# Performance work log

Hardware: AMD Instinct MI355X
Metric: run time of the kernel (lower is better)

Reference implementation:

```python
import jax, jax.numpy as jnp
import numpy as np

B, C, H, W = 16, 256, 32, 32
K = 8192            # codebook_size
COMMITMENT = 0.25   # commitment_cost


def setup_inputs() -> dict:
    key = jax.random.key(0)
    k1, k2 = jax.random.split(key)
    z = jax.random.normal(k1, (B, C, H, W), dtype=jnp.float32)
    # matches nn.init.uniform_(codebook.weight, -1/K, 1/K)
    codebook = jax.random.uniform(k2, (K, C), dtype=jnp.float32,
                                  minval=-1.0 / K, maxval=1.0 / K)
    return {"z": z, "codebook": codebook}


def reference(z, codebook):
    b, c, h, w = z.shape
    # (B, C, H, W) -> (B, H*W, C)
    z_flat = z.transpose(0, 2, 3, 1).reshape(b, h * w, c)
    # squared euclidean distances; argmin of sq-dist == argmin of cdist
    z_sq = jnp.sum(z_flat * z_flat, axis=-1, keepdims=True)        # (B, N, 1)
    e_sq = jnp.sum(codebook * codebook, axis=-1)                   # (K,)
    cross = jnp.einsum('bnc,kc->bnk', z_flat, codebook)            # (B, N, K)
    distances = z_sq - 2.0 * cross + e_sq                          # (B, N, K)
    codes = jnp.argmin(distances, axis=-1)                         # (B, N)
    quantized = codebook[codes]                                    # (B, N, C)
    codebook_loss = jnp.mean((quantized - jax.lax.stop_gradient(z_flat)) ** 2)
    commitment_loss = jnp.mean((z_flat - jax.lax.stop_gradient(quantized)) ** 2)
    vq_loss = codebook_loss + COMMITMENT * commitment_loss
    # straight-through estimator
    quantized_st = z_flat + jax.lax.stop_gradient(quantized - z_flat)
    codes_out = codes.reshape(b, h, w)
    quantized_out = quantized_st.reshape(b, h, w, c).transpose(0, 3, 1, 2)
    return codes_out, quantized_out, vq_loss
```

## Files before the change

### kernel.cpp

```cpp
#include <hip/hip_runtime.h>


typedef _Float16 f16;
typedef __attribute__((ext_vector_type(8))) _Float16 f16x8;
typedef __attribute__((ext_vector_type(4))) float f32x4;

#define NPIX   16384
#define CDIM   256
#define KCODE  8192

__global__ void k_prep(const float* __restrict__ z, const float* __restrict__ cb,
                       f16* __restrict__ zhi, f16* __restrict__ zlo,
                       float* __restrict__ zsq,
                       f16* __restrict__ bfh, f16* __restrict__ bfl,
                       float* __restrict__ esq) {
  int bid = blockIdx.x;
  int t   = threadIdx.x;
  if (bid < 512) {
    int kb = bid;
#pragma unroll
    for (int half = 0; half < 2; ++half) {
      int o    = half * 256 + t;
      int lane = o & 63;
      int cs   = o >> 6;
      int code = kb * 16 + (lane & 15);
      int c0   = cs * 32 + ((lane >> 4) & 3) * 8;
      const float* src = cb + (size_t)code * CDIM + c0;
      float4 v0 = *(const float4*)(src);
      float4 v1 = *(const float4*)(src + 4);
      float e[8] = {v0.x, v0.y, v0.z, v0.w, v1.x, v1.y, v1.z, v1.w};
      f16x8 h8, l8;
#pragma unroll
      for (int j = 0; j < 8; ++j) {
        float ej = e[j] * 8192.0f;
        f16 h = (f16)ej;
        h8[j] = h;
        l8[j] = (f16)((ej - (float)h) * 4096.0f);
      }
      size_t off = ((size_t)kb * 512 + o) * 8;
      *(f16x8*)(bfh + off) = h8;
      *(f16x8*)(bfl + off) = l8;
    }
  } else if (bid < 576) {
#pragma clang fp contract(off)
    int n = (bid - 512) * 256 + t;
    int b = n >> 10, p = n & 1023;
    const float* src = z + (size_t)b * CDIM * 1024 + p;
    f16* dh = zhi + (size_t)n * CDIM;
    f16* dl = zlo + (size_t)n * CDIM;
    float half_[2];
    for (int m = 0; m < 2; ++m) {
      float r[8];
#pragma unroll
      for (int j = 0; j < 8; ++j) r[j] = 0.0f;
      for (int i = 0; i < 16; ++i) {
        f16x8 h8, l8;
#pragma unroll
        for (int j = 0; j < 8; ++j) {
          float v = src[(size_t)(m * 128 + i * 8 + j) * 1024];
          r[j] = r[j] + v * v;
          f16 h = (f16)v;
          h8[j] = h;
          l8[j] = (f16)((v - (float)h) * 4096.0f);
        }
        *(f16x8*)(dh + m * 128 + i * 8) = h8;
        *(f16x8*)(dl + m * 128 + i * 8) = l8;
      }
      half_[m] = ((r[0] + r[1]) + (r[2] + r[3])) + ((r[4] + r[5]) + (r[6] + r[7]));
    }
    zsq[n] = half_[0] + half_[1];
  } else {
#pragma clang fp contract(off)
    int row = (bid - 576) * 256 + t;
    const float* src = cb + (size_t)row * CDIM;
    float half_[2];
    for (int m = 0; m < 2; ++m) {
      float r[8];
#pragma unroll
      for (int j = 0; j < 8; ++j) r[j] = 0.0f;
      for (int i = 0; i < 16; ++i) {
        float4 v0 = *(const float4*)(src + m * 128 + i * 8);
        float4 v1 = *(const float4*)(src + m * 128 + i * 8 + 4);
        r[0] = r[0] + v0.x * v0.x;  r[1] = r[1] + v0.y * v0.y;
        r[2] = r[2] + v0.z * v0.z;  r[3] = r[3] + v0.w * v0.w;
        r[4] = r[4] + v1.x * v1.x;  r[5] = r[5] + v1.y * v1.y;
        r[6] = r[6] + v1.z * v1.z;  r[7] = r[7] + v1.w * v1.w;
      }
      half_[m] = ((r[0] + r[1]) + (r[2] + r[3])) + ((r[4] + r[5]) + (r[6] + r[7]));
    }
    esq[row] = half_[0] + half_[1];
  }
}

#define LOADB(Bset, it) do {                                                  \
    int kbq_ = kslice * 64 + (it) * 2 + wk;                                   \
    size_t base_ = (size_t)kbq_ * 4096 + (size_t)lane * 8;                    \
    _Pragma("unroll")                                                         \
    for (int cs_ = 0; cs_ < 8; ++cs_) {                                       \
      Bset[2*cs_]   = *(const f16x8*)(bfh + base_ + (size_t)cs_ * 512);       \
      Bset[2*cs_+1] = *(const f16x8*)(bfl + base_ + (size_t)cs_ * 512);       \
    } } while (0)

#define COMPUTE(Bset, it) do {                                                \
    int kbase_ = kslice * 1024 + (it) * 32 + wk * 16;                         \
    f32x4 hh[2], mx[2];                                                       \
    _Pragma("unroll")                                                         \
    for (int rt = 0; rt < 2; ++rt) { hh[rt] = vzero; mx[rt] = vzero; }        \
    _Pragma("unroll")                                                         \
    for (int cs = 0; cs < 8; ++cs) {                                          \
      f16x8 ah[2], al[2];                                                     \
      _Pragma("unroll")                                                       \
      for (int rt = 0; rt < 2; ++rt) {                                        \
        int px = wh * 32 + rt * 16 + l15;                                     \
        int sb = (cs * 4 + quad) ^ (px & 7);                                  \
        int eo = px * 256 + sb * 8;                            \
        ah[rt] = *(const f16x8*)(sAh + eo);                                   \
        al[rt] = *(const f16x8*)(sAl + eo);                                   \
      }                                                                       \
      _Pragma("unroll")                                                       \
      for (int rt = 0; rt < 2; ++rt) {                                        \
        hh[rt] = __builtin_amdgcn_mfma_f32_16x16x32_f16(ah[rt], Bset[2*cs],   hh[rt], 0, 0, 0); \
        mx[rt] = __builtin_amdgcn_mfma_f32_16x16x32_f16(ah[rt], Bset[2*cs+1], mx[rt], 0, 0, 0); \
        mx[rt] = __builtin_amdgcn_mfma_f32_16x16x32_f16(al[rt], Bset[2*cs],   mx[rt], 0, 0, 0); \
      }                                                                       \
    }                                                                         \
    {                                                                         \
      int k = kbase_ + l15;                                                   \
      float es = esq[k];                                                      \
      _Pragma("unroll")                                                       \
      for (int rt = 0; rt < 2; ++rt)                                          \
        _Pragma("unroll")                                                     \
        for (int rr = 0; rr < 4; ++rr) {                                      \
          float v = hh[rt][rr] * 2.44140625e-4f;                   \
          float w = fmaf(mx[rt][rr], 5.9604644775390625e-8f, v);              \
          float d = (Zr[rt * 4 + rr] - w) + es;                               \
          int j = rt * 4 + rr;                                                \
          if (d < bs[j]) { bs[j] = d; bi[j] = k; }                            \
        }                                                                     \
    } } while (0)

__launch_bounds__(256)
__global__ void k_score(const f16* __restrict__ bfh, const f16* __restrict__ bfl,
                        const f16* __restrict__ zhi, const f16* __restrict__ zlo,
                        const float* __restrict__ esq, const float* __restrict__ zsq,
                        int* __restrict__ cnt,
                        unsigned long long* __restrict__ best) {
  extern __shared__ char smem[];
  f16* sAh = (f16*)smem;
  f16* sAl = (f16*)(smem + 32768);
  int t = threadIdx.x;
  int wave = t >> 6, lane = t & 63;
  int quad = lane >> 4, l15 = lane & 15;
  int wh = wave & 1;
  int wk = wave >> 1;

  __shared__ int s_job[2];
  if (t == 0) {
    unsigned xcc;
    asm volatile("s_getreg_b32 %0, hwreg(HW_REG_XCC_ID)" : "=s"(xcc));
    int x = (int)(xcc & 7u);
    int pt = -1, ks = 0;
    for (int trial = 0; trial < 16 && pt < 0; ++trial) {
      int j = (x + trial) & 7;
      int tk = atomicAdd(&cnt[j], 1);
      if (tk < 256) { pt = tk; ks = j; }
    }
    if (pt < 0) pt = 0;
    s_job[0] = pt; s_job[1] = ks;
  }
  __syncthreads();
  int ptile  = s_job[0];
  int kslice = s_job[1];
  int p0 = ptile * 64;

  {
    int r = t >> 2, seg = t & 3;
    const uint4* gh = (const uint4*)zhi + ((size_t)(p0 + r)) * 32;
    const uint4* gl = (const uint4*)zlo + ((size_t)(p0 + r)) * 32;
    uint4* sh = (uint4*)sAh + r * 32;
    uint4* sl = (uint4*)sAl + r * 32;
#pragma unroll
    for (int j = 0; j < 8; ++j) {
      int blk = seg * 8 + j;
      int sb = blk ^ (r & 7);
      sh[sb] = gh[blk];
      sl[sb] = gl[blk];
    }
  }

  float Zr[8];
#pragma unroll
  for (int rt = 0; rt < 2; ++rt)
#pragma unroll
    for (int rr = 0; rr < 4; ++rr)
      Zr[rt * 4 + rr] = zsq[p0 + wh * 32 + rt * 16 + quad * 4 + rr];

  __syncthreads();

  float bs[8];
  int   bi[8];
#pragma unroll
  for (int j = 0; j < 8; ++j) { bs[j] = 3.0e38f; bi[j] = 0; }

  const f32x4 vzero = {0.0f, 0.0f, 0.0f, 0.0f};

  f16x8 B0[16], B1[16];
  LOADB(B0, 0);
#pragma unroll 1
  for (int tt = 0; tt < 16; ++tt) {
    int i0 = tt * 2, i1 = tt * 2 + 1;
    LOADB(B1, i1);
    COMPUTE(B0, i0);
    int inext = (i1 + 1 < 32) ? i1 + 1 : 31;
    LOADB(B0, inext);
    COMPUTE(B1, i1);
  }

  __syncthreads();
  unsigned long long* red = (unsigned long long*)smem;
#pragma unroll
  for (int j = 0; j < 8; ++j) {
    float s = bs[j]; int i_ = bi[j];
#pragma unroll
    for (int m = 1; m <= 8; m <<= 1) {
      float s2 = __shfl_xor(s, m);
      int   i2 = __shfl_xor(i_, m);
      if (s2 < s || (s2 == s && i2 < i_)) { s = s2; i_ = i2; }
    }
    if (l15 == 0) {
      int row32 = ((j >> 2) << 4) + (quad << 2) + (j & 3);
      unsigned u = __float_as_uint(s);
      u = (u & 0x80000000u) ? ~u : (u | 0x80000000u);
      red[wave * 32 + row32] = ((unsigned long long)u << 32) | (unsigned)i_;
    }
  }
  __syncthreads();
  if (wave == 0) {
    int wh2 = lane >> 5, r31 = lane & 31;
    unsigned long long a = red[wh2 * 32 + r31];
    unsigned long long b = red[(wh2 + 2) * 32 + r31];
    if (b < a) a = b;
    atomicMin(&best[p0 + lane], a);
  }
}

__global__ void k_gather(const float* __restrict__ z, const float* __restrict__ cb,
                         const unsigned long long* __restrict__ best,
                         float* __restrict__ out_codes, float* __restrict__ out_q,
                         float* __restrict__ lossac) {
  int b  = blockIdx.x >> 4;
  int cg = blockIdx.x & 15;
  int t  = threadIdx.x;
  int idx[4];
#pragma unroll
  for (int pi = 0; pi < 4; ++pi) {
    int p = t + pi * 256;
    unsigned long long pk = best[b * 1024 + p];
    idx[pi] = (int)(unsigned)(pk & 0xffffffffu);
    if (cg == 0) out_codes[b * 1024 + p] = (float)idx[pi];
  }
  float lsum = 0.0f;
#pragma unroll
  for (int ci = 0; ci < 16; ++ci) {
    int c = cg * 16 + ci;
#pragma unroll
    for (int pi = 0; pi < 4; ++pi) {
      int p = t + pi * 256;
      float q  = cb[(size_t)idx[pi] * CDIM + c];
      size_t o = ((size_t)(b * CDIM + c)) * 1024 + p;
      float zv = z[o];
      float d  = q - zv;
      out_q[o] = zv + d;
      lsum = fmaf(d, d, lsum);
    }
  }
#pragma unroll
  for (int m = 32; m >= 1; m >>= 1) lsum += __shfl_xor(lsum, m);
  __shared__ float wsum[4];
  if ((t & 63) == 0) wsum[t >> 6] = lsum;
  __syncthreads();
  if (t == 0) atomicAdd(lossac, wsum[0] + wsum[1] + wsum[2] + wsum[3]);
}

__global__ void k_final(const float* __restrict__ lossac, float* __restrict__ out_loss) {
  if (threadIdx.x == 0) out_loss[0] = lossac[0] * (1.25f / 4194304.0f);
}

extern "C" void kernel_launch(void* const* d_in, const int* in_sizes, int n_in,
                              void* d_out, int out_size, void* d_ws, size_t ws_size,
                              hipStream_t stream) {
  (void)in_sizes; (void)n_in; (void)out_size; (void)ws_size;
  const float* z  = (const float*)d_in[0];
  const float* cb = (const float*)d_in[1];
  float* outf = (float*)d_out;

  char* ws = (char*)d_ws;
  f16*   bfh  = (f16*)ws;
  f16*   bfl  = (f16*)(ws + (4 << 20));
  float* esq  = (float*)(ws + (8 << 20));
  unsigned long long* best = (unsigned long long*)(ws + (8 << 20) + 32768);
  float* lossac = (float*)(ws + (8 << 20) + 32768 + 131072);
  float* zsq    = (float*)(ws + (8 << 20) + 32768 + 131072 + 256);
  int*   cnt    = (int*)  (ws + (8 << 20) + 32768 + 131072 + 256 + 65536);

  f16* zhi = (f16*)(outf + 16384);
  f16* zlo = zhi + (size_t)NPIX * CDIM;

  hipMemsetAsync(best, 0xFF, (size_t)NPIX * 8, stream);
  hipMemsetAsync(lossac, 0, 4, stream);
  hipMemsetAsync(cnt, 0, 32, stream);

  k_prep   <<<608,  256, 0,     stream>>>(z, cb, zhi, zlo, zsq, bfh, bfl, esq);
  k_score  <<<2048, 256, 65536, stream>>>(bfh, bfl, zhi, zlo, esq, zsq, cnt, best);
  k_gather <<<256,  256, 0,     stream>>>(z, cb, best, outf, outf + 16384, lossac);
  k_final  <<<1,    64,  0,     stream>>>(lossac, outf + 16384 + (size_t)NPIX * CDIM);
}
```

Measured before the change: 349.7 us.

## Fold memsets into prep kernel and hoist first A-tile fragments into registers

Drops three hipMemsetAsync calls by adding an extra block to k_prep that initializes the best array, the loss accumulator and the counters, which removes separate launch overhead. In k_score, the A fragments for the first 16-row tile are loaded from LDS once into registers before the main loop, instead of being reloaded on every iteration, which cuts LDS traffic. The cost is 16 extra f16x8 registers per thread, which may lower occupancy or cause spills alongside the double-buffered B registers.

```diff
diff --git a/kernel.cpp b/kernel.cpp
--- a/kernel.cpp
+++ b/kernel.cpp
@@ -13,7 +13,9 @@
                        f16* __restrict__ zhi, f16* __restrict__ zlo,
                        float* __restrict__ zsq,
                        f16* __restrict__ bfh, f16* __restrict__ bfl,
-                       float* __restrict__ esq) {
+                       float* __restrict__ esq,
+                       unsigned long long* __restrict__ best,
+                       float* __restrict__ lossac, int* __restrict__ cnt) {
   int bid = blockIdx.x;
   int t   = threadIdx.x;
   if (bid < 512) {
@@ -69,7 +71,7 @@
       half_[m] = ((r[0] + r[1]) + (r[2] + r[3])) + ((r[4] + r[5]) + (r[6] + r[7]));
     }
     zsq[n] = half_[0] + half_[1];
-  } else {
+  } else if (bid < 608) {
 #pragma clang fp contract(off)
     int row = (bid - 576) * 256 + t;
     const float* src = cb + (size_t)row * CDIM;
@@ -89,6 +91,12 @@
       half_[m] = ((r[0] + r[1]) + (r[2] + r[3])) + ((r[4] + r[5]) + (r[6] + r[7]));
     }
     esq[row] = half_[0] + half_[1];
+  } else {
+#pragma unroll 4
+    for (int i = 0; i < 64; ++i)
+      best[(size_t)i * 256 + t] = ~0ull;
+    if (t == 0) *lossac = 0.0f;
+    if (t < 8) cnt[t] = 0;
   }
 }
 
@@ -108,21 +116,20 @@
     for (int rt = 0; rt < 2; ++rt) { hh[rt] = vzero; mx[rt] = vzero; }        \
     _Pragma("unroll")                                                         \
     for (int cs = 0; cs < 8; ++cs) {                                          \
-      f16x8 ah[2], al[2];                                                     \
-      _Pragma("unroll")                                                       \
-      for (int rt = 0; rt < 2; ++rt) {                                        \
-        int px = wh * 32 + rt * 16 + l15;                                     \
+      f16x8 ah1, al1;                                                         \
+      {                                                                       \
+        int px = wh * 32 + 16 + l15;                                          \
         int sb = (cs * 4 + quad) ^ (px & 7);                                  \
         int eo = px * 256 + sb * 8;                            \
-        ah[rt] = *(const f16x8*)(sAh + eo);                                   \
-        al[rt] = *(const f16x8*)(sAl + eo);                                   \
+        ah1 = *(const f16x8*)(sAh + eo);                                      \
+        al1 = *(const f16x8*)(sAl + eo);                                      \
       }                                                                       \
-      _Pragma("unroll")                                                       \
-      for (int rt = 0; rt < 2; ++rt) {                                        \
-        hh[rt] = __builtin_amdgcn_mfma_f32_16x16x32_f16(ah[rt], Bset[2*cs],   hh[rt], 0, 0, 0); \
-        mx[rt] = __builtin_amdgcn_mfma_f32_16x16x32_f16(ah[rt], Bset[2*cs+1], mx[rt], 0, 0, 0); \
-        mx[rt] = __builtin_amdgcn_mfma_f32_16x16x32_f16(al[rt], Bset[2*cs],   mx[rt], 0, 0, 0); \
-      }                                                                       \
+      hh[0] = __builtin_amdgcn_mfma_f32_16x16x32_f16(aA0[2*cs],   Bset[2*cs],   hh[0], 0, 0, 0); \
+      mx[0] = __builtin_amdgcn_mfma_f32_16x16x32_f16(aA0[2*cs],   Bset[2*cs+1], mx[0], 0, 0, 0); \
+      mx[0] = __builtin_amdgcn_mfma_f32_16x16x32_f16(aA0[2*cs+1], Bset[2*cs],   mx[0], 0, 0, 0); \
+      hh[1] = __builtin_amdgcn_mfma_f32_16x16x32_f16(ah1,         Bset[2*cs],   hh[1], 0, 0, 0); \
+      mx[1] = __builtin_amdgcn_mfma_f32_16x16x32_f16(ah1,         Bset[2*cs+1], mx[1], 0, 0, 0); \
+      mx[1] = __builtin_amdgcn_mfma_f32_16x16x32_f16(al1,         Bset[2*cs],   mx[1], 0, 0, 0); \
     }                                                                         \
     {                                                                         \
       int k = kbase_ + l15;                                                   \
@@ -197,6 +204,16 @@
 
   __syncthreads();
 
+  f16x8 aA0[16];
+#pragma unroll
+  for (int cs = 0; cs < 8; ++cs) {
+    int px = wh * 32 + l15;
+    int sb = (cs * 4 + quad) ^ (px & 7);
+    int eo = px * 256 + sb * 8;
+    aA0[2*cs]   = *(const f16x8*)(sAh + eo);
+    aA0[2*cs+1] = *(const f16x8*)(sAl + eo);
+  }
+
   float bs[8];
   int   bi[8];
 #pragma unroll
@@ -306,11 +323,8 @@
   f16* zhi = (f16*)(outf + 16384);
   f16* zlo = zhi + (size_t)NPIX * CDIM;
 
-  hipMemsetAsync(best, 0xFF, (size_t)NPIX * 8, stream);
-  hipMemsetAsync(lossac, 0, 4, stream);
-  hipMemsetAsync(cnt, 0, 32, stream);
-
-  k_prep   <<<608,  256, 0,     stream>>>(z, cb, zhi, zlo, zsq, bfh, bfl, esq);
+  k_prep   <<<609,  256, 0,     stream>>>(z, cb, zhi, zlo, zsq, bfh, bfl, esq,
+                                          best, lossac, cnt);
   k_score  <<<2048, 256, 65536, stream>>>(bfh, bfl, zhi, zlo, esq, zsq, cnt, best);
   k_gather <<<256,  256, 0,     stream>>>(z, cb, best, outf, outf + 16384, lossac);
   k_final  <<<1,    64,  0,     stream>>>(lossac, outf + 16384 + (size_t)NPIX * CDIM);
```

Result: no change. 345.9 us (-1.1%).

## Double k_score pixel tile to 128 and fold memsets into prep kernel

Applied to the files above, without the earlier changes.

The scoring kernel now runs 512-thread blocks over 128-pixel tiles with a 128 KB static LDS buffer, replacing 256-thread blocks over 64 pixels. Each block reuses every streamed codebook fragment across twice as many pixels, which halves global codebook traffic per pixel. The job counter limit and the final per-row atomicMin reduction are adjusted to match the new wave layout. The three hipMemsetAsync calls are replaced by an extra block in the prep kernel that initialises best, lossac and cnt, removing separate launches. The trade-off is one block per CU with a large LDS footprint and fewer blocks to balance across CUs.

```diff
diff --git a/kernel.cpp b/kernel.cpp
--- a/kernel.cpp
+++ b/kernel.cpp
@@ -13,7 +13,9 @@
                        f16* __restrict__ zhi, f16* __restrict__ zlo,
                        float* __restrict__ zsq,
                        f16* __restrict__ bfh, f16* __restrict__ bfl,
-                       float* __restrict__ esq) {
+                       float* __restrict__ esq,
+                       unsigned long long* __restrict__ best,
+                       float* __restrict__ lossac, int* __restrict__ cnt) {
   int bid = blockIdx.x;
   int t   = threadIdx.x;
   if (bid < 512) {
@@ -69,7 +71,7 @@
       half_[m] = ((r[0] + r[1]) + (r[2] + r[3])) + ((r[4] + r[5]) + (r[6] + r[7]));
     }
     zsq[n] = half_[0] + half_[1];
-  } else {
+  } else if (bid < 608) {
 #pragma clang fp contract(off)
     int row = (bid - 576) * 256 + t;
     const float* src = cb + (size_t)row * CDIM;
@@ -89,6 +91,12 @@
       half_[m] = ((r[0] + r[1]) + (r[2] + r[3])) + ((r[4] + r[5]) + (r[6] + r[7]));
     }
     esq[row] = half_[0] + half_[1];
+  } else {
+#pragma unroll 4
+    for (int i = 0; i < 64; ++i)
+      best[(size_t)i * 256 + t] = ~0ull;
+    if (t == 0) *lossac = 0.0f;
+    if (t < 8) cnt[t] = 0;
   }
 }
 
@@ -139,20 +147,20 @@
         }                                                                     \
     } } while (0)
 
-__launch_bounds__(256)
+__launch_bounds__(512)
 __global__ void k_score(const f16* __restrict__ bfh, const f16* __restrict__ bfl,
                         const f16* __restrict__ zhi, const f16* __restrict__ zlo,
                         const float* __restrict__ esq, const float* __restrict__ zsq,
                         int* __restrict__ cnt,
                         unsigned long long* __restrict__ best) {
-  extern __shared__ char smem[];
+  __shared__ __align__(16) char smem[131072];
   f16* sAh = (f16*)smem;
-  f16* sAl = (f16*)(smem + 32768);
+  f16* sAl = (f16*)(smem + 65536);
   int t = threadIdx.x;
   int wave = t >> 6, lane = t & 63;
   int quad = lane >> 4, l15 = lane & 15;
-  int wh = wave & 1;
-  int wk = wave >> 1;
+  int wh = wave >> 1;
+  int wk = wave & 1;
 
   __shared__ int s_job[2];
   if (t == 0) {
@@ -163,7 +171,7 @@
     for (int trial = 0; trial < 16 && pt < 0; ++trial) {
       int j = (x + trial) & 7;
       int tk = atomicAdd(&cnt[j], 1);
-      if (tk < 256) { pt = tk; ks = j; }
+      if (tk < 128) { pt = tk; ks = j; }
     }
     if (pt < 0) pt = 0;
     s_job[0] = pt; s_job[1] = ks;
@@ -171,7 +179,7 @@
   __syncthreads();
   int ptile  = s_job[0];
   int kslice = s_job[1];
-  int p0 = ptile * 64;
+  int p0 = ptile * 128;
 
   {
     int r = t >> 2, seg = t & 3;
@@ -236,11 +244,15 @@
   }
   __syncthreads();
   if (wave == 0) {
-    int wh2 = lane >> 5, r31 = lane & 31;
-    unsigned long long a = red[wh2 * 32 + r31];
-    unsigned long long b = red[(wh2 + 2) * 32 + r31];
-    if (b < a) a = b;
-    atomicMin(&best[p0 + lane], a);
+#pragma unroll
+    for (int half = 0; half < 2; ++half) {
+      int r = half * 64 + lane;
+      int wh2 = r >> 5, r32 = r & 31;
+      unsigned long long a = red[(wh2 * 2 + 0) * 32 + r32];
+      unsigned long long b = red[(wh2 * 2 + 1) * 32 + r32];
+      if (b < a) a = b;
+      atomicMin(&best[p0 + r], a);
+    }
   }
 }
 
@@ -306,12 +318,9 @@
   f16* zhi = (f16*)(outf + 16384);
   f16* zlo = zhi + (size_t)NPIX * CDIM;
 
-  hipMemsetAsync(best, 0xFF, (size_t)NPIX * 8, stream);
-  hipMemsetAsync(lossac, 0, 4, stream);
-  hipMemsetAsync(cnt, 0, 32, stream);
-
-  k_prep   <<<608,  256, 0,     stream>>>(z, cb, zhi, zlo, zsq, bfh, bfl, esq);
-  k_score  <<<2048, 256, 65536, stream>>>(bfh, bfl, zhi, zlo, esq, zsq, cnt, best);
-  k_gather <<<256,  256, 0,     stream>>>(z, cb, best, outf, outf + 16384, lossac);
-  k_final  <<<1,    64,  0,     stream>>>(lossac, outf + 16384 + (size_t)NPIX * CDIM);
-}
+  k_prep   <<<609,  256, 0, stream>>>(z, cb, zhi, zlo, zsq, bfh, bfl, esq,
+                                      best, lossac, cnt);
+  k_score  <<<1024, 512, 0, stream>>>(bfh, bfl, zhi, zlo, esq, zsq, cnt, best);
+  k_gather <<<256,  256, 0, stream>>>(z, cb, best, outf, outf + 16384, lossac);
+  k_final  <<<1,    64,  0, stream>>>(lossac, outf + 16384 + (size_t)NPIX * CDIM);
+}
```

Measured after the change: 369.7 us. 1.06x slower.
